# Performance work log

Hardware: AMD Instinct MI355X
Metric: run time of the kernel (lower is better)

Reference implementation:

```python
import jax, jax.numpy as jnp
import numpy as np

SCALE = 0.08838834764831845  # 1/sqrt(head_dim=128)


def setup_inputs() -> dict:
    key = jax.random.key(0)
    ks = jax.random.split(key, 5)
    B, H, D = 16, 8, 128          # batch (decode seqs), kv heads, head_dim
    BS, BPS = 16, 128             # block_size, blocks per sequence
    NBLK = B * BPS                # total cache blocks (2048)
    CTX = 2048                    # context length per sequence
    q = jax.random.normal(ks[0], (B, H, D), jnp.float32)
    k = jax.random.normal(ks[1], (B, H, D), jnp.float32)
    v = jax.random.normal(ks[2], (B, H, D), jnp.float32)
    k_cache = jax.random.normal(ks[3], (NBLK, BS, H, D), jnp.float32)
    v_cache = jax.random.normal(ks[4], (NBLK, BS, H, D), jnp.float32)
    # each sequence owns a distinct contiguous set of blocks
    block_tables = jnp.arange(B * BPS, dtype=jnp.int32).reshape(B, BPS)
    context_lens = jnp.full((B,), CTX, dtype=jnp.int32)
    # slot for the newest token (position CTX-1) of each sequence
    last = CTX - 1
    slot_mapping = block_tables[:, last // BS] * BS + (last % BS)
    return {"q": q, "k": k, "v": v, "k_cache": k_cache, "v_cache": v_cache,
            "slot_mapping": slot_mapping.astype(jnp.int32),
            "block_tables": block_tables, "context_lens": context_lens}


def reference(q, k, v, k_cache, v_cache, slot_mapping, block_tables, context_lens):
    # ---- store_kvcache: scatter new k/v tokens into paged caches ----
    nblk, bs, H, D = k_cache.shape
    k_cache = k_cache.reshape(nblk * bs, H, D).at[slot_mapping].set(k).reshape(nblk, bs, H, D)
    v_cache = v_cache.reshape(nblk * bs, H, D).at[slot_mapping].set(v).reshape(nblk, bs, H, D)

    # ---- _sdpa_decode: paged gather + masked attention (q_per_seq = 1) ----
    B, nb = block_tables.shape
    T = nb * bs                              # max tokens per sequence
    token_idx = jnp.arange(T, dtype=jnp.int32)
    block_idx = token_idx // bs
    token_off = token_idx % bs
    block_ids = block_tables[:, block_idx]   # [B, T]
    k_all = k_cache[block_ids, token_off]    # [B, T, H, D]
    v_all = v_cache[block_ids, token_off]    # [B, T, H, D]

    valid = token_idx[None, :] < context_lens[:, None]           # [B, T]
    q_pos = context_lens - 1                                     # q_per_seq == 1
    causal = token_idx[None, :] <= q_pos[:, None]                # [B, T]
    mask = valid & causal

    scores = jnp.einsum("bhd,bthd->bht", q, k_all) * SCALE       # [B, H, T]
    scores = jnp.where(mask[:, None, :], scores, -jnp.inf)
    p = jax.nn.softmax(scores, axis=-1)
    out = jnp.einsum("bht,bthd->bhd", p, v_all)                  # [B, H, D]
    return out
```

## Files before the change

kernel.cpp:

```cpp
#include <hip/hip_runtime.h>
#include <math.h>

#define B_ 16
#define H_ 8
#define D_ 128
#define BS_ 16
#define BPS_ 128
#define T_ (BPS_ * BS_)
#define ROW_ (H_ * D_)
#define SCALE_ 0.08838834764831845f

template<int NS>
__global__ __launch_bounds__(256, 4) void attn_partial(
    const float* __restrict__ q,
    const float* __restrict__ knew,
    const float* __restrict__ vnew,
    const float* __restrict__ kc,
    const float* __restrict__ vc,
    const int* __restrict__ btab,
    const int* __restrict__ clen,
    float* __restrict__ ws_m,
    float* __restrict__ ws_l,
    float* __restrict__ ws_o)
{
    constexpr int CHUNK = T_ / NS;
    constexpr int TPW = CHUNK / 4;
    static_assert(TPW % 4 == 0 || TPW == 4, "TPW multiple of 4");
    constexpr int NB = TPW / 4;

    const int c = blockIdx.x;
    const int b = blockIdx.y;
    const int tid = threadIdx.x;
    const int wave = tid >> 6;
    const int lane = tid & 63;
    const int h = lane >> 3;
    const int e = (lane & 7) * 4;
    const int ctx = clen[b];
    const int cs = c * CHUNK;
    const int t0 = wave * TPW;

    __shared__ float s_p[H_][CHUNK + 1];
    __shared__ float s_mx[H_], s_l[H_];
    __shared__ float s_o[4][H_ * D_];

    float4 q4[4];
    #pragma unroll
    for (int i = 0; i < 4; ++i)
        q4[i] = *(const float4*)(q + (size_t)b * ROW_ + h * 128 + i * 32 + e);

    float sc[TPW];

    #pragma unroll
    for (int bt = 0; bt < NB; ++bt) {
        float4 kb[4][4];
        #pragma unroll
        for (int u = 0; u < 4; ++u) {
            const int t = t0 + bt * 4 + u;
            const int tg = cs + t;
            const int blk = btab[b * BPS_ + (tg >> 4)];
            const float* rb = (tg == ctx - 1)
                ? (knew + (size_t)b * ROW_)
                : (kc + ((size_t)blk * BS_ + (t & 15)) * ROW_);
            #pragma unroll
            for (int i = 0; i < 4; ++i)
                kb[u][i] = *(const float4*)(rb + h * 128 + i * 32 + e);
        }
        #pragma unroll
        for (int u = 0; u < 4; ++u) {
            const int t = t0 + bt * 4 + u;
            const int tg = cs + t;
            float s = 0.f;
            #pragma unroll
            for (int i = 0; i < 4; ++i)
                s += q4[i].x * kb[u][i].x + q4[i].y * kb[u][i].y
                   + q4[i].z * kb[u][i].z + q4[i].w * kb[u][i].w;
            s += __shfl_xor(s, 1);
            s += __shfl_xor(s, 2);
            s += __shfl_xor(s, 4);
            s = (tg < ctx) ? s * SCALE_ : -INFINITY;
            sc[bt * 4 + u] = s;
            if ((lane & 7) == 0) s_p[h][t] = s;
        }
    }

    float4 vb0[4][4];
    #pragma unroll
    for (int u = 0; u < 4; ++u) {
        const int t = t0 + u;
        const int tg = cs + t;
        const int blk = btab[b * BPS_ + (tg >> 4)];
        const float* rb = (tg == ctx - 1)
            ? (vnew + (size_t)b * ROW_)
            : (vc + ((size_t)blk * BS_ + (t & 15)) * ROW_);
        #pragma unroll
        for (int i = 0; i < 4; ++i)
            vb0[u][i] = *(const float4*)(rb + h * 128 + i * 32 + e);
    }

    asm volatile("s_waitcnt lgkmcnt(0)" ::: "memory");
    __builtin_amdgcn_s_barrier();
    __builtin_amdgcn_sched_barrier(0);

    {
        const int hh = tid >> 5;
        const int j = tid & 31;
        float m = -INFINITY;
        for (int t = j; t < CHUNK; t += 32) m = fmaxf(m, s_p[hh][t]);
        m = fmaxf(m, __shfl_xor(m, 16));
        m = fmaxf(m, __shfl_xor(m, 8));
        m = fmaxf(m, __shfl_xor(m, 4));
        m = fmaxf(m, __shfl_xor(m, 2));
        m = fmaxf(m, __shfl_xor(m, 1));
        m = fmaxf(m, -1e30f);
        float l = 0.f;
        for (int t = j; t < CHUNK; t += 32) l += __expf(s_p[hh][t] - m);
        l += __shfl_xor(l, 16);
        l += __shfl_xor(l, 8);
        l += __shfl_xor(l, 4);
        l += __shfl_xor(l, 2);
        l += __shfl_xor(l, 1);
        if (j == 0) { s_mx[hh] = m; s_l[hh] = l; }
    }

    asm volatile("s_waitcnt lgkmcnt(0)" ::: "memory");
    __builtin_amdgcn_s_barrier();
    __builtin_amdgcn_sched_barrier(0);

    const float mx = s_mx[h];

    float4 acc[4];
    #pragma unroll
    for (int i = 0; i < 4; ++i) acc[i] = make_float4(0.f, 0.f, 0.f, 0.f);

    #pragma unroll
    for (int u = 0; u < 4; ++u) {
        const float pw = __expf(sc[u] - mx);
        #pragma unroll
        for (int i = 0; i < 4; ++i) {
            acc[i].x += pw * vb0[u][i].x;
            acc[i].y += pw * vb0[u][i].y;
            acc[i].z += pw * vb0[u][i].z;
            acc[i].w += pw * vb0[u][i].w;
        }
    }
    #pragma unroll
    for (int bt = 1; bt < NB; ++bt) {
        float4 vb[4][4];
        #pragma unroll
        for (int u = 0; u < 4; ++u) {
            const int t = t0 + bt * 4 + u;
            const int tg = cs + t;
            const int blk = btab[b * BPS_ + (tg >> 4)];
            const float* rb = (tg == ctx - 1)
                ? (vnew + (size_t)b * ROW_)
                : (vc + ((size_t)blk * BS_ + (t & 15)) * ROW_);
            #pragma unroll
            for (int i = 0; i < 4; ++i)
                vb[u][i] = *(const float4*)(rb + h * 128 + i * 32 + e);
        }
        #pragma unroll
        for (int u = 0; u < 4; ++u) {
            const float pw = __expf(sc[bt * 4 + u] - mx);
            #pragma unroll
            for (int i = 0; i < 4; ++i) {
                acc[i].x += pw * vb[u][i].x;
                acc[i].y += pw * vb[u][i].y;
                acc[i].z += pw * vb[u][i].z;
                acc[i].w += pw * vb[u][i].w;
            }
        }
    }

    #pragma unroll
    for (int i = 0; i < 4; ++i)
        *(float4*)&s_o[wave][h * 128 + i * 32 + e] = acc[i];

    asm volatile("s_waitcnt lgkmcnt(0)" ::: "memory");
    __builtin_amdgcn_s_barrier();
    __builtin_amdgcn_sched_barrier(0);

    for (int r = tid; r < H_ * D_; r += 256) {
        const float oo = s_o[0][r] + s_o[1][r] + s_o[2][r] + s_o[3][r];
        ws_o[((size_t)(b * H_ + (r >> 7)) * NS + c) * D_ + (r & 127)] = oo;
    }
    if (tid < H_) {
        ws_m[(b * H_ + tid) * NS + c] = s_mx[tid];
        ws_l[(b * H_ + tid) * NS + c] = s_l[tid];
    }
}

template<int NS>
__global__ __launch_bounds__(128) void attn_reduce(
    const float* __restrict__ ws_m,
    const float* __restrict__ ws_l,
    const float* __restrict__ ws_o,
    float* __restrict__ out)
{
    const int bh = blockIdx.x;
    const int tid = threadIdx.x;

    __shared__ float s_co[NS];
    __shared__ float s_lg;

    if (tid < 64) {
        float m = -INFINITY;
        for (int cc = tid; cc < NS; cc += 64) m = fmaxf(m, ws_m[bh * NS + cc]);
        m = fmaxf(m, __shfl_xor(m, 32));
        m = fmaxf(m, __shfl_xor(m, 16));
        m = fmaxf(m, __shfl_xor(m, 8));
        m = fmaxf(m, __shfl_xor(m, 4));
        m = fmaxf(m, __shfl_xor(m, 2));
        m = fmaxf(m, __shfl_xor(m, 1));
        float lw = 0.f;
        for (int cc = tid; cc < NS; cc += 64) {
            const float co = __expf(ws_m[bh * NS + cc] - m);
            s_co[cc] = co;
            lw += ws_l[bh * NS + cc] * co;
        }
        lw += __shfl_xor(lw, 32);
        lw += __shfl_xor(lw, 16);
        lw += __shfl_xor(lw, 8);
        lw += __shfl_xor(lw, 4);
        lw += __shfl_xor(lw, 2);
        lw += __shfl_xor(lw, 1);
        if (tid == 0) s_lg = lw;
    }
    __syncthreads();

    float acc = 0.f;
    #pragma unroll 8
    for (int cc = 0; cc < NS; ++cc)
        acc += s_co[cc] * ws_o[((size_t)bh * NS + cc) * D_ + tid];
    out[(size_t)bh * D_ + tid] = acc / s_lg;
}

template<int NS>
static void launch_all(const float* q, const float* knew, const float* vnew,
                       const float* kc, const float* vc,
                       const int* btab, const int* clen,
                       float* ws, float* out, hipStream_t stream)
{
    float* ws_m = ws;
    float* ws_l = ws + B_ * H_ * NS;
    float* ws_o = ws + 2 * B_ * H_ * NS;
    attn_partial<NS><<<dim3(NS, B_), 256, 0, stream>>>(q, knew, vnew, kc, vc,
                                                       btab, clen, ws_m, ws_l, ws_o);
    attn_reduce<NS><<<dim3(B_ * H_), 128, 0, stream>>>(ws_m, ws_l, ws_o, out);
}

extern "C" void kernel_launch(void* const* d_in, const int* in_sizes, int n_in,
                              void* d_out, int out_size, void* d_ws, size_t ws_size,
                              hipStream_t stream) {
    const float* q    = (const float*)d_in[0];
    const float* knew = (const float*)d_in[1];
    const float* vnew = (const float*)d_in[2];
    const float* kc   = (const float*)d_in[3];
    const float* vc   = (const float*)d_in[4];
    const int* btab = (const int*)d_in[6];
    const int* clen = (const int*)d_in[7];
    float* out = (float*)d_out;
    float* ws  = (float*)d_ws;

    const size_t need128 = (size_t)B_ * H_ * 128 * (2 + D_) * sizeof(float);
    const size_t need64  = (size_t)B_ * H_ * 64  * (2 + D_) * sizeof(float);
    const size_t need32  = (size_t)B_ * H_ * 32  * (2 + D_) * sizeof(float);
    if (ws_size >= need128)     launch_all<128>(q, knew, vnew, kc, vc, btab, clen, ws, out, stream);
    else if (ws_size >= need64) launch_all<64>(q, knew, vnew, kc, vc, btab, clen, ws, out, stream);
    else if (ws_size >= need32) launch_all<32>(q, knew, vnew, kc, vc, btab, clen, ws, out, stream);
    else                        launch_all<16>(q, knew, vnew, kc, vc, btab, clen, ws, out, stream);
}
```

Before: 296.7 us.

## Use single-wave blocks with register softmax and finer sequence split

Partial attention blocks shrink from four waves to one wave. Each wave now keeps all chunk scores in registers and computes the max and sum locally, which removes the shared-memory score/output staging and all block barriers. The split count rises to 256 when the workspace permits, so there are more, smaller blocks. In exchange, the partial-output workspace and the reduce kernel's work grow.

Measured after the change: 305.0 us. 2.8% more time.

```diff
diff --git a/kernel.cpp b/kernel.cpp
--- a/kernel.cpp
+++ b/kernel.cpp
@@ -11,7 +11,7 @@
 #define SCALE_ 0.08838834764831845f
 
 template<int NS>
-__global__ __launch_bounds__(256, 4) void attn_partial(
+__global__ __launch_bounds__(64, 4) void attn_partial(
     const float* __restrict__ q,
     const float* __restrict__ knew,
     const float* __restrict__ vnew,
@@ -24,51 +24,41 @@
     float* __restrict__ ws_o)
 {
     constexpr int CHUNK = T_ / NS;
-    constexpr int TPW = CHUNK / 4;
-    static_assert(TPW % 4 == 0 || TPW == 4, "TPW multiple of 4");
-    constexpr int NB = TPW / 4;
+    constexpr int NB = CHUNK / 4;
+    static_assert(CHUNK % 4 == 0, "CHUNK multiple of 4");
 
     const int c = blockIdx.x;
     const int b = blockIdx.y;
-    const int tid = threadIdx.x;
-    const int wave = tid >> 6;
-    const int lane = tid & 63;
+    const int lane = threadIdx.x;
     const int h = lane >> 3;
     const int e = (lane & 7) * 4;
     const int ctx = clen[b];
     const int cs = c * CHUNK;
-    const int t0 = wave * TPW;
-
-    __shared__ float s_p[H_][CHUNK + 1];
-    __shared__ float s_mx[H_], s_l[H_];
-    __shared__ float s_o[4][H_ * D_];
 
     float4 q4[4];
     #pragma unroll
     for (int i = 0; i < 4; ++i)
         q4[i] = *(const float4*)(q + (size_t)b * ROW_ + h * 128 + i * 32 + e);
 
-    float sc[TPW];
+    float sc[CHUNK];
 
     #pragma unroll
     for (int bt = 0; bt < NB; ++bt) {
         float4 kb[4][4];
         #pragma unroll
         for (int u = 0; u < 4; ++u) {
-            const int t = t0 + bt * 4 + u;
-            const int tg = cs + t;
+            const int tg = cs + bt * 4 + u;
             const int blk = btab[b * BPS_ + (tg >> 4)];
             const float* rb = (tg == ctx - 1)
                 ? (knew + (size_t)b * ROW_)
-                : (kc + ((size_t)blk * BS_ + (t & 15)) * ROW_);
+                : (kc + ((size_t)blk * BS_ + (tg & 15)) * ROW_);
             #pragma unroll
             for (int i = 0; i < 4; ++i)
                 kb[u][i] = *(const float4*)(rb + h * 128 + i * 32 + e);
         }
         #pragma unroll
         for (int u = 0; u < 4; ++u) {
-            const int t = t0 + bt * 4 + u;
-            const int tg = cs + t;
+            const int tg = cs + bt * 4 + u;
             float s = 0.f;
             #pragma unroll
             for (int i = 0; i < 4; ++i)
@@ -77,90 +67,42 @@
             s += __shfl_xor(s, 1);
             s += __shfl_xor(s, 2);
             s += __shfl_xor(s, 4);
-            s = (tg < ctx) ? s * SCALE_ : -INFINITY;
-            sc[bt * 4 + u] = s;
-            if ((lane & 7) == 0) s_p[h][t] = s;
-        }
-    }
-
-    float4 vb0[4][4];
-    #pragma unroll
-    for (int u = 0; u < 4; ++u) {
-        const int t = t0 + u;
-        const int tg = cs + t;
-        const int blk = btab[b * BPS_ + (tg >> 4)];
-        const float* rb = (tg == ctx - 1)
-            ? (vnew + (size_t)b * ROW_)
-            : (vc + ((size_t)blk * BS_ + (t & 15)) * ROW_);
-        #pragma unroll
-        for (int i = 0; i < 4; ++i)
-            vb0[u][i] = *(const float4*)(rb + h * 128 + i * 32 + e);
-    }
-
-    asm volatile("s_waitcnt lgkmcnt(0)" ::: "memory");
-    __builtin_amdgcn_s_barrier();
-    __builtin_amdgcn_sched_barrier(0);
-
-    {
-        const int hh = tid >> 5;
-        const int j = tid & 31;
-        float m = -INFINITY;
-        for (int t = j; t < CHUNK; t += 32) m = fmaxf(m, s_p[hh][t]);
-        m = fmaxf(m, __shfl_xor(m, 16));
-        m = fmaxf(m, __shfl_xor(m, 8));
-        m = fmaxf(m, __shfl_xor(m, 4));
-        m = fmaxf(m, __shfl_xor(m, 2));
-        m = fmaxf(m, __shfl_xor(m, 1));
-        m = fmaxf(m, -1e30f);
-        float l = 0.f;
-        for (int t = j; t < CHUNK; t += 32) l += __expf(s_p[hh][t] - m);
-        l += __shfl_xor(l, 16);
-        l += __shfl_xor(l, 8);
-        l += __shfl_xor(l, 4);
-        l += __shfl_xor(l, 2);
-        l += __shfl_xor(l, 1);
-        if (j == 0) { s_mx[hh] = m; s_l[hh] = l; }
-    }
-
-    asm volatile("s_waitcnt lgkmcnt(0)" ::: "memory");
-    __builtin_amdgcn_s_barrier();
-    __builtin_amdgcn_sched_barrier(0);
-
-    const float mx = s_mx[h];
+            sc[bt * 4 + u] = (tg < ctx) ? s * SCALE_ : -INFINITY;
+        }
+    }
+
+    float m = -INFINITY;
+    #pragma unroll
+    for (int t = 0; t < CHUNK; ++t) m = fmaxf(m, sc[t]);
+    m = fmaxf(m, -1e30f);
+    float l = 0.f;
+    #pragma unroll
+    for (int t = 0; t < CHUNK; ++t) {
+        sc[t] = __expf(sc[t] - m);
+        l += sc[t];
+    }
 
     float4 acc[4];
     #pragma unroll
     for (int i = 0; i < 4; ++i) acc[i] = make_float4(0.f, 0.f, 0.f, 0.f);
 
     #pragma unroll
-    for (int u = 0; u < 4; ++u) {
-        const float pw = __expf(sc[u] - mx);
-        #pragma unroll
-        for (int i = 0; i < 4; ++i) {
-            acc[i].x += pw * vb0[u][i].x;
-            acc[i].y += pw * vb0[u][i].y;
-            acc[i].z += pw * vb0[u][i].z;
-            acc[i].w += pw * vb0[u][i].w;
-        }
-    }
-    #pragma unroll
-    for (int bt = 1; bt < NB; ++bt) {
+    for (int bt = 0; bt < NB; ++bt) {
         float4 vb[4][4];
         #pragma unroll
         for (int u = 0; u < 4; ++u) {
-            const int t = t0 + bt * 4 + u;
-            const int tg = cs + t;
+            const int tg = cs + bt * 4 + u;
             const int blk = btab[b * BPS_ + (tg >> 4)];
             const float* rb = (tg == ctx - 1)
                 ? (vnew + (size_t)b * ROW_)
-                : (vc + ((size_t)blk * BS_ + (t & 15)) * ROW_);
+                : (vc + ((size_t)blk * BS_ + (tg & 15)) * ROW_);
             #pragma unroll
             for (int i = 0; i < 4; ++i)
                 vb[u][i] = *(const float4*)(rb + h * 128 + i * 32 + e);
         }
         #pragma unroll
         for (int u = 0; u < 4; ++u) {
-            const float pw = __expf(sc[bt * 4 + u] - mx);
+            const float pw = sc[bt * 4 + u];
             #pragma unroll
             for (int i = 0; i < 4; ++i) {
                 acc[i].x += pw * vb[u][i].x;
@@ -173,19 +115,10 @@
 
     #pragma unroll
     for (int i = 0; i < 4; ++i)
-        *(float4*)&s_o[wave][h * 128 + i * 32 + e] = acc[i];
-
-    asm volatile("s_waitcnt lgkmcnt(0)" ::: "memory");
-    __builtin_amdgcn_s_barrier();
-    __builtin_amdgcn_sched_barrier(0);
-
-    for (int r = tid; r < H_ * D_; r += 256) {
-        const float oo = s_o[0][r] + s_o[1][r] + s_o[2][r] + s_o[3][r];
-        ws_o[((size_t)(b * H_ + (r >> 7)) * NS + c) * D_ + (r & 127)] = oo;
-    }
-    if (tid < H_) {
-        ws_m[(b * H_ + tid) * NS + c] = s_mx[tid];
-        ws_l[(b * H_ + tid) * NS + c] = s_l[tid];
+        *(float4*)(ws_o + ((size_t)(b * H_ + h) * NS + c) * D_ + i * 32 + e) = acc[i];
+    if ((lane & 7) == 0) {
+        ws_m[(b * H_ + h) * NS + c] = m;
+        ws_l[(b * H_ + h) * NS + c] = l;
     }
 }
 
@@ -243,8 +176,8 @@
     float* ws_m = ws;
     float* ws_l = ws + B_ * H_ * NS;
     float* ws_o = ws + 2 * B_ * H_ * NS;
-    attn_partial<NS><<<dim3(NS, B_), 256, 0, stream>>>(q, knew, vnew, kc, vc,
-                                                       btab, clen, ws_m, ws_l, ws_o);
+    attn_partial<NS><<<dim3(NS, B_), 64, 0, stream>>>(q, knew, vnew, kc, vc,
+                                                      btab, clen, ws_m, ws_l, ws_o);
     attn_reduce<NS><<<dim3(B_ * H_), 128, 0, stream>>>(ws_m, ws_l, ws_o, out);
 }
 
@@ -261,11 +194,10 @@
     float* out = (float*)d_out;
     float* ws  = (float*)d_ws;
 
+    const size_t need256 = (size_t)B_ * H_ * 256 * (2 + D_) * sizeof(float);
     const size_t need128 = (size_t)B_ * H_ * 128 * (2 + D_) * sizeof(float);
     const size_t need64  = (size_t)B_ * H_ * 64  * (2 + D_) * sizeof(float);
-    const size_t need32  = (size_t)B_ * H_ * 32  * (2 + D_) * sizeof(float);
-    if (ws_size >= need128)     launch_all<128>(q, knew, vnew, kc, vc, btab, clen, ws, out, stream);
-    else if (ws_size >= need64) launch_all<64>(q, knew, vnew, kc, vc, btab, clen, ws, out, stream);
-    else if (ws_size >= need32) launch_all<32>(q, knew, vnew, kc, vc, btab, clen, ws, out, stream);
-    else                        launch_all<16>(q, knew, vnew, kc, vc, btab, clen, ws, out, stream);
-}
+    if (ws_size >= need256)     launch_all<256>(q, knew, vnew, kc, vc, btab, clen, ws, out, stream);
+    else if (ws_size >= need128) launch_all<128>(q, knew, vnew, kc, vc, btab, clen, ws, out, stream);
+    else                         launch_all<64>(q, knew, vnew, kc, vc, btab, clen, ws, out, stream);
+}
```
